# Optimization experiments

Measured on AMD Instinct MI355X. Metric: run time of the kernel, lower is better.

The kernel has to match this reference:

```python
import jax, jax.numpy as jnp
import numpy as np

F, H, D, A, B = 500, 2000, 64, 64, 4096


def setup_inputs() -> dict:
    key = jax.random.key(0)
    ks = jax.random.split(key, 6)
    values = jax.random.normal(ks[0], (B, F), dtype=jnp.float32)
    feat_emb = jax.random.normal(ks[1], (F, D), dtype=jnp.float32) * 0.02
    hid_emb = jax.random.normal(ks[2], (H, D), dtype=jnp.float32) * 0.02
    Ww = jax.random.normal(ks[3], (2 * D, A), dtype=jnp.float32) * (1.0 / np.sqrt(2 * D))
    bw = jnp.zeros((A,), dtype=jnp.float32)
    Wu = jax.random.normal(ks[4], (A, 1), dtype=jnp.float32) * (1.0 / np.sqrt(A))
    mask = jax.random.bernoulli(ks[5], 0.1, (F, F + H, 1))
    return {"values": values, "feat_emb": feat_emb, "hid_emb": hid_emb,
            "Ww": Ww, "bw": bw, "Wu": Wu, "mask": mask}


def reference(values, feat_emb, hid_emb, Ww, bw, Wu, mask):
    d = feat_emb.shape[1]
    # full embedding matrix: concat(feature, hidden) -> [F+H, d]
    full = jnp.concatenate([feat_emb, hid_emb], axis=0)
    # Dense(tanh) on concat([feat_emb tiled, full tiled], axis=2) == split-weight form:
    # avoids materializing the [F, F+H, 2d] concat tensor (same math).
    W1, W2 = Ww[:d], Ww[d:]
    pre_f = feat_emb @ W1          # [F, A]
    pre_w = full @ W2              # [F+H, A]
    h = jnp.tanh(pre_f[:, None, :] + pre_w[None, :, :] + bw)  # [F, F+H, A]
    score = h @ Wu                 # [F, F+H, 1]
    # masked exp-normalize (not a stable softmax: original uses raw exp)
    score = jnp.where(mask, jnp.exp(score), 0.0)
    ssum = jnp.sum(score, axis=1, keepdims=True)        # [F, 1, 1]
    ssum = jnp.where(ssum == 0, 1.0, ssum)
    attn = score / ssum                                  # [F, F+H, 1]
    context = jnp.sum(attn * full[None, :, :], axis=1)   # [F, d]
    return values @ context                              # [B, d]
```

## Files before the change

### kernel.cpp

```cpp
#include <hip/hip_runtime.h>
#include <cstdint>
#include <cstddef>

#define F_N 500
#define H_N 2000
#define JN  2500
#define D_N 64
#define A_N 64
#define B_N 4096

__global__ __launch_bounds__(256) void k_pre(
    const float* __restrict__ feat, const float* __restrict__ hid,
    const float* __restrict__ Ww,   const float* __restrict__ bw,
    float* __restrict__ pre_f, float* __restrict__ pre_w)
{
    const int lane = threadIdx.x & 63;
    const int wave = threadIdx.x >> 6;
    int row = blockIdx.x * 4 + wave;
    row = __builtin_amdgcn_readfirstlane(row);
    if (row >= F_N + JN) return;

    const float* emb;
    const float* W;
    float*       outp;
    float acc0, acc1 = 0.0f;

    if (row < F_N) {
        emb  = feat + (size_t)row * D_N;
        W    = Ww;
        outp = pre_f + (size_t)row * A_N;
        acc0 = bw[lane];
    } else {
        const int j = row - F_N;
        emb  = (j < F_N) ? (feat + (size_t)j * D_N)
                         : (hid + (size_t)(j - F_N) * D_N);
        W    = Ww + D_N * A_N;
        outp = pre_w + (size_t)j * A_N;
        acc0 = 0.0f;
    }

    #pragma unroll
    for (int d = 0; d < D_N; d += 2) {
        acc0 = fmaf(emb[d],     W[(d    ) * A_N + lane], acc0);
        acc1 = fmaf(emb[d + 1], W[(d + 1) * A_N + lane], acc1);
    }
    outp[lane] = acc0 + acc1;
}

__global__ __launch_bounds__(256) void k_attn(
    const float* __restrict__ feat, const float* __restrict__ hid,
    const float* __restrict__ pre_f, const float* __restrict__ pre_w,
    const float* __restrict__ Wu,   const void* __restrict__ mask,
    float* __restrict__ ctx)
{
    const int tid  = threadIdx.x;
    const int lane = tid & 63;
    const int wave = tid >> 6;
    const int i    = blockIdx.x;

    __shared__ int   list[JN];
    __shared__ float earr[JN];
    __shared__ float s_ctx[4][64];
    __shared__ int   nact;

    if (tid == 0) nact = 0;
    __syncthreads();

    const uint32_t* mw = (const uint32_t*)mask;
    const uint32_t probe = mw[lane] | mw[64 + lane] | mw[128 + lane] | mw[192 + lane];
    const bool byteMode = (__ballot(probe > 1u) != 0ull);

    const uint8_t*  mb = (const uint8_t*)mask + (size_t)i * JN;
    const uint32_t* mi = (const uint32_t*)mask + (size_t)i * JN;

    for (int t = tid; t < 2560; t += 256) {
        uint32_t m = 0;
        if (t < JN) m = byteMode ? (uint32_t)mb[t] : mi[t];
        const unsigned long long act = __ballot(m != 0);
        const int cnt = __popcll(act);
        int base = 0;
        if (lane == 0 && cnt) base = atomicAdd(&nact, cnt);
        base = __shfl(base, 0, 64);
        if (m) {
            const int rank = __popcll(act & ((1ull << lane) - 1ull));
            list[base + rank] = t;
        }
    }
    __syncthreads();
    const int n = nact;

    const float* pf = pre_f + (size_t)i * A_N;
    for (int idx = tid; idx < n; idx += 256) {
        const int j = list[idx];
        const float4* pwj = (const float4*)(pre_w + (size_t)j * A_N);
        float s = 0.0f;
        #pragma unroll
        for (int q = 0; q < 16; ++q) {
            const float4 v = pwj[q];
            const int a = q * 4;
            const float x0 = pf[a + 0] + v.x;
            const float x1 = pf[a + 1] + v.y;
            const float x2 = pf[a + 2] + v.z;
            const float x3 = pf[a + 3] + v.w;
            const float t0 = 1.0f - 2.0f / (__expf(2.0f * x0) + 1.0f);
            const float t1 = 1.0f - 2.0f / (__expf(2.0f * x1) + 1.0f);
            const float t2 = 1.0f - 2.0f / (__expf(2.0f * x2) + 1.0f);
            const float t3 = 1.0f - 2.0f / (__expf(2.0f * x3) + 1.0f);
            s = fmaf(Wu[a + 0], t0, s);
            s = fmaf(Wu[a + 1], t1, s);
            s = fmaf(Wu[a + 2], t2, s);
            s = fmaf(Wu[a + 3], t3, s);
        }
        earr[idx] = __expf(s);
    }
    __syncthreads();

    float cacc = 0.0f;
    int idx = wave;
    for (; idx + 12 < n; idx += 16) {
        const float e0 = earr[idx];      const int j0 = list[idx];
        const float e1 = earr[idx + 4];  const int j1 = list[idx + 4];
        const float e2 = earr[idx + 8];  const int j2 = list[idx + 8];
        const float e3 = earr[idx + 12]; const int j3 = list[idx + 12];
        const float* r0 = (j0 < F_N) ? (feat + (size_t)j0 * D_N) : (hid + (size_t)(j0 - F_N) * D_N);
        const float* r1 = (j1 < F_N) ? (feat + (size_t)j1 * D_N) : (hid + (size_t)(j1 - F_N) * D_N);
        const float* r2 = (j2 < F_N) ? (feat + (size_t)j2 * D_N) : (hid + (size_t)(j2 - F_N) * D_N);
        const float* r3 = (j3 < F_N) ? (feat + (size_t)j3 * D_N) : (hid + (size_t)(j3 - F_N) * D_N);
        const float v0 = r0[lane];
        const float v1 = r1[lane];
        const float v2 = r2[lane];
        const float v3 = r3[lane];
        cacc = fmaf(e0, v0, cacc);
        cacc = fmaf(e1, v1, cacc);
        cacc = fmaf(e2, v2, cacc);
        cacc = fmaf(e3, v3, cacc);
    }
    for (; idx < n; idx += 4) {
        const float e = earr[idx];
        const int   j = list[idx];
        const float* row = (j < F_N) ? (feat + (size_t)j * D_N)
                                     : (hid + (size_t)(j - F_N) * D_N);
        cacc = fmaf(e, row[lane], cacc);
    }
    s_ctx[wave][lane] = cacc;
    __syncthreads();

    if (wave == 0) {
        const float c4 = s_ctx[0][lane] + s_ctx[1][lane] + s_ctx[2][lane] + s_ctx[3][lane];
        float ss = 0.0f;
        for (int k = lane; k < n; k += 64) ss += earr[k];
        #pragma unroll
        for (int off = 1; off < 64; off <<= 1) ss += __shfl_xor(ss, off, 64);
        if (ss == 0.0f) ss = 1.0f;
        ctx[(size_t)i * D_N + lane] = c4 / ss;
    }
}

__global__ __launch_bounds__(256) void k_out(
    const float* __restrict__ values, const float* __restrict__ ctx,
    float* __restrict__ out)
{
    const int tid  = threadIdx.x;
    const int lane = tid & 63;
    const int wave = tid >> 6;
    const int rowB = blockIdx.x * 16;
    const int r0   = wave * 4;

    __shared__ float ctx_l[100 * 64];
    __shared__ float vals_l[16 * 100];

    float4 cbuf[7];
    float4 vbuf[2];

    float acc0 = 0.0f, acc1 = 0.0f, acc2 = 0.0f, acc3 = 0.0f;

    {
        const float4* cp = (const float4*)(ctx);
        #pragma unroll
        for (int q = 0; q < 7; ++q) {
            const int t = tid + q * 256;
            if (t < 1600) cbuf[q] = cp[t];
        }
        #pragma unroll
        for (int q = 0; q < 2; ++q) {
            const int t = tid + q * 256;
            if (t < 400) {
                const int r = t / 25, c = t % 25;
                vbuf[q] = *(const float4*)(values + (size_t)(rowB + r) * 500 + c * 4);
            }
        }
    }

    for (int chunk = 0; chunk < 5; ++chunk) {
        __syncthreads();
        {
            float4* cl = (float4*)ctx_l;
            #pragma unroll
            for (int q = 0; q < 7; ++q) {
                const int t = tid + q * 256;
                if (t < 1600) cl[t] = cbuf[q];
            }
            float4* vl = (float4*)vals_l;
            #pragma unroll
            for (int q = 0; q < 2; ++q) {
                const int t = tid + q * 256;
                if (t < 400) vl[t] = vbuf[q];
            }
        }
        __syncthreads();

        if (chunk < 4) {
            const int k0 = (chunk + 1) * 100;
            const float4* cp = (const float4*)(ctx + (size_t)k0 * 64);
            #pragma unroll
            for (int q = 0; q < 7; ++q) {
                const int t = tid + q * 256;
                if (t < 1600) cbuf[q] = cp[t];
            }
            #pragma unroll
            for (int q = 0; q < 2; ++q) {
                const int t = tid + q * 256;
                if (t < 400) {
                    const int r = t / 25, c = t % 25;
                    vbuf[q] = *(const float4*)(values + (size_t)(rowB + r) * 500 + k0 + c * 4);
                }
            }
        }

        const float* v0 = vals_l + (r0 + 0) * 100;
        const float* v1 = vals_l + (r0 + 1) * 100;
        const float* v2 = vals_l + (r0 + 2) * 100;
        const float* v3 = vals_l + (r0 + 3) * 100;
        #pragma unroll 5
        for (int k = 0; k < 100; k += 4) {
            const float4 a = *(const float4*)(v0 + k);
            const float4 b = *(const float4*)(v1 + k);
            const float4 c = *(const float4*)(v2 + k);
            const float4 d = *(const float4*)(v3 + k);
            const float c0 = ctx_l[(k + 0) * 64 + lane];
            const float c1 = ctx_l[(k + 1) * 64 + lane];
            const float c2 = ctx_l[(k + 2) * 64 + lane];
            const float c3 = ctx_l[(k + 3) * 64 + lane];
            acc0 = fmaf(a.x, c0, acc0); acc0 = fmaf(a.y, c1, acc0);
            acc0 = fmaf(a.z, c2, acc0); acc0 = fmaf(a.w, c3, acc0);
            acc1 = fmaf(b.x, c0, acc1); acc1 = fmaf(b.y, c1, acc1);
            acc1 = fmaf(b.z, c2, acc1); acc1 = fmaf(b.w, c3, acc1);
            acc2 = fmaf(c.x, c0, acc2); acc2 = fmaf(c.y, c1, acc2);
            acc2 = fmaf(c.z, c2, acc2); acc2 = fmaf(c.w, c3, acc2);
            acc3 = fmaf(d.x, c0, acc3); acc3 = fmaf(d.y, c1, acc3);
            acc3 = fmaf(d.z, c2, acc3); acc3 = fmaf(d.w, c3, acc3);
        }
    }

    const int gr = rowB + r0;
    out[(size_t)(gr + 0) * 64 + lane] = acc0;
    out[(size_t)(gr + 1) * 64 + lane] = acc1;
    out[(size_t)(gr + 2) * 64 + lane] = acc2;
    out[(size_t)(gr + 3) * 64 + lane] = acc3;
}

extern "C" void kernel_launch(void* const* d_in, const int* in_sizes, int n_in,
                              void* d_out, int out_size, void* d_ws, size_t ws_size,
                              hipStream_t stream)
{
    const float* values = (const float*)d_in[0];
    const float* feat   = (const float*)d_in[1];
    const float* hid    = (const float*)d_in[2];
    const float* Ww     = (const float*)d_in[3];
    const float* bw     = (const float*)d_in[4];
    const float* Wu     = (const float*)d_in[5];
    const void*  mask   = d_in[6];
    float* out = (float*)d_out;

    float* wsf   = (float*)d_ws;
    float* pre_f = wsf;
    float* pre_w = wsf + 32000;
    float* ctx   = wsf + 192000;

    k_pre <<<750, 256, 0, stream>>>(feat, hid, Ww, bw, pre_f, pre_w);
    k_attn<<<500, 256, 0, stream>>>(feat, hid, pre_f, pre_w, Wu, mask, ctx);
    k_out <<<256, 256, 0, stream>>>(values, ctx, out);
}
```

Baseline: 129.3 us.

## Fuse attention and output kernels with a software grid barrier

Merges the attention-context kernel and the final values@context kernel into one persistent launch of 256 blocks. The first 250 blocks each handle two feature rows, then a spin-based global barrier waits until all of ctx is written before the output GEMM phase starts. The barrier counter is reset by the preceding k_pre kernel. The tanh division is also replaced by a hardware reciprocal. This removes one launch and its inter-kernel gap, but it halves the parallelism of the attention phase, adds barrier spin cost, and relies on all 256 blocks being co-resident.

```diff
diff --git a/kernel.cpp b/kernel.cpp
--- a/kernel.cpp
+++ b/kernel.cpp
@@ -8,12 +8,16 @@
 #define D_N 64
 #define A_N 64
 #define B_N 4096
+#define NB_FUSED 256
 
 __global__ __launch_bounds__(256) void k_pre(
     const float* __restrict__ feat, const float* __restrict__ hid,
     const float* __restrict__ Ww,   const float* __restrict__ bw,
-    float* __restrict__ pre_f, float* __restrict__ pre_w)
+    float* __restrict__ pre_f, float* __restrict__ pre_w,
+    int* __restrict__ barrier_ws)
 {
+    if (blockIdx.x == 0 && threadIdx.x < 2) barrier_ws[threadIdx.x] = 0;
+
     const int lane = threadIdx.x & 63;
     const int wave = threadIdx.x >> 6;
     int row = blockIdx.x * 4 + wave;
@@ -47,171 +51,160 @@
     outp[lane] = acc0 + acc1;
 }
 
-__global__ __launch_bounds__(256) void k_attn(
+__device__ __forceinline__ void grid_barrier(int* __restrict__ ctr,
+                                             int* __restrict__ gen,
+                                             int nblocks)
+{
+    __syncthreads();
+    if (threadIdx.x == 0) {
+        __threadfence();
+        const int g = __hip_atomic_load(gen, __ATOMIC_RELAXED,
+                                        __HIP_MEMORY_SCOPE_AGENT);
+        const int old = __hip_atomic_fetch_add(ctr, 1, __ATOMIC_ACQ_REL,
+                                               __HIP_MEMORY_SCOPE_AGENT);
+        if (old == nblocks - 1) {
+            __hip_atomic_store(gen, g + 1, __ATOMIC_RELEASE,
+                               __HIP_MEMORY_SCOPE_AGENT);
+        } else {
+            while (__hip_atomic_load(gen, __ATOMIC_ACQUIRE,
+                                     __HIP_MEMORY_SCOPE_AGENT) == g) {
+                __builtin_amdgcn_s_sleep(2);
+            }
+        }
+    }
+    __syncthreads();
+}
+
+__global__ __launch_bounds__(256) void k_fused(
     const float* __restrict__ feat, const float* __restrict__ hid,
     const float* __restrict__ pre_f, const float* __restrict__ pre_w,
     const float* __restrict__ Wu,   const void* __restrict__ mask,
-    float* __restrict__ ctx)
+    const float* __restrict__ values,
+    float* __restrict__ ctx, float* __restrict__ out,
+    int* __restrict__ barrier_ws)
 {
     const int tid  = threadIdx.x;
     const int lane = tid & 63;
     const int wave = tid >> 6;
-    const int i    = blockIdx.x;
 
     __shared__ int   list[JN];
     __shared__ float earr[JN];
     __shared__ float s_ctx[4][64];
     __shared__ int   nact;
-
-    if (tid == 0) nact = 0;
-    __syncthreads();
-
-    const uint32_t* mw = (const uint32_t*)mask;
-    const uint32_t probe = mw[lane] | mw[64 + lane] | mw[128 + lane] | mw[192 + lane];
-    const bool byteMode = (__ballot(probe > 1u) != 0ull);
-
-    const uint8_t*  mb = (const uint8_t*)mask + (size_t)i * JN;
-    const uint32_t* mi = (const uint32_t*)mask + (size_t)i * JN;
-
-    for (int t = tid; t < 2560; t += 256) {
-        uint32_t m = 0;
-        if (t < JN) m = byteMode ? (uint32_t)mb[t] : mi[t];
-        const unsigned long long act = __ballot(m != 0);
-        const int cnt = __popcll(act);
-        int base = 0;
-        if (lane == 0 && cnt) base = atomicAdd(&nact, cnt);
-        base = __shfl(base, 0, 64);
-        if (m) {
-            const int rank = __popcll(act & ((1ull << lane) - 1ull));
-            list[base + rank] = t;
-        }
-    }
-    __syncthreads();
-    const int n = nact;
-
-    const float* pf = pre_f + (size_t)i * A_N;
-    for (int idx = tid; idx < n; idx += 256) {
-        const int j = list[idx];
-        const float4* pwj = (const float4*)(pre_w + (size_t)j * A_N);
-        float s = 0.0f;
-        #pragma unroll
-        for (int q = 0; q < 16; ++q) {
-            const float4 v = pwj[q];
-            const int a = q * 4;
-            const float x0 = pf[a + 0] + v.x;
-            const float x1 = pf[a + 1] + v.y;
-            const float x2 = pf[a + 2] + v.z;
-            const float x3 = pf[a + 3] + v.w;
-            const float t0 = 1.0f - 2.0f / (__expf(2.0f * x0) + 1.0f);
-            const float t1 = 1.0f - 2.0f / (__expf(2.0f * x1) + 1.0f);
-            const float t2 = 1.0f - 2.0f / (__expf(2.0f * x2) + 1.0f);
-            const float t3 = 1.0f - 2.0f / (__expf(2.0f * x3) + 1.0f);
-            s = fmaf(Wu[a + 0], t0, s);
-            s = fmaf(Wu[a + 1], t1, s);
-            s = fmaf(Wu[a + 2], t2, s);
-            s = fmaf(Wu[a + 3], t3, s);
-        }
-        earr[idx] = __expf(s);
-    }
-    __syncthreads();
-
-    float cacc = 0.0f;
-    int idx = wave;
-    for (; idx + 12 < n; idx += 16) {
-        const float e0 = earr[idx];      const int j0 = list[idx];
-        const float e1 = earr[idx + 4];  const int j1 = list[idx + 4];
-        const float e2 = earr[idx + 8];  const int j2 = list[idx + 8];
-        const float e3 = earr[idx + 12]; const int j3 = list[idx + 12];
-        const float* r0 = (j0 < F_N) ? (feat + (size_t)j0 * D_N) : (hid + (size_t)(j0 - F_N) * D_N);
-        const float* r1 = (j1 < F_N) ? (feat + (size_t)j1 * D_N) : (hid + (size_t)(j1 - F_N) * D_N);
-        const float* r2 = (j2 < F_N) ? (feat + (size_t)j2 * D_N) : (hid + (size_t)(j2 - F_N) * D_N);
-        const float* r3 = (j3 < F_N) ? (feat + (size_t)j3 * D_N) : (hid + (size_t)(j3 - F_N) * D_N);
-        const float v0 = r0[lane];
-        const float v1 = r1[lane];
-        const float v2 = r2[lane];
-        const float v3 = r3[lane];
-        cacc = fmaf(e0, v0, cacc);
-        cacc = fmaf(e1, v1, cacc);
-        cacc = fmaf(e2, v2, cacc);
-        cacc = fmaf(e3, v3, cacc);
-    }
-    for (; idx < n; idx += 4) {
-        const float e = earr[idx];
-        const int   j = list[idx];
-        const float* row = (j < F_N) ? (feat + (size_t)j * D_N)
-                                     : (hid + (size_t)(j - F_N) * D_N);
-        cacc = fmaf(e, row[lane], cacc);
-    }
-    s_ctx[wave][lane] = cacc;
-    __syncthreads();
-
-    if (wave == 0) {
-        const float c4 = s_ctx[0][lane] + s_ctx[1][lane] + s_ctx[2][lane] + s_ctx[3][lane];
-        float ss = 0.0f;
-        for (int k = lane; k < n; k += 64) ss += earr[k];
-        #pragma unroll
-        for (int off = 1; off < 64; off <<= 1) ss += __shfl_xor(ss, off, 64);
-        if (ss == 0.0f) ss = 1.0f;
-        ctx[(size_t)i * D_N + lane] = c4 / ss;
-    }
-}
-
-__global__ __launch_bounds__(256) void k_out(
-    const float* __restrict__ values, const float* __restrict__ ctx,
-    float* __restrict__ out)
-{
-    const int tid  = threadIdx.x;
-    const int lane = tid & 63;
-    const int wave = tid >> 6;
-    const int rowB = blockIdx.x * 16;
-    const int r0   = wave * 4;
-
     __shared__ float ctx_l[100 * 64];
     __shared__ float vals_l[16 * 100];
 
-    float4 cbuf[7];
-    float4 vbuf[2];
-
-    float acc0 = 0.0f, acc1 = 0.0f, acc2 = 0.0f, acc3 = 0.0f;
+    if (blockIdx.x < 250) {
+        const uint32_t* mw = (const uint32_t*)mask;
+        const uint32_t probe = mw[lane] | mw[64 + lane] | mw[128 + lane] | mw[192 + lane];
+        const bool byteMode = (__ballot(probe > 1u) != 0ull);
+
+        for (int rep = 0; rep < 2; ++rep) {
+            const int i = blockIdx.x * 2 + rep;
+
+            if (tid == 0) nact = 0;
+            __syncthreads();
+
+            const uint8_t*  mb = (const uint8_t*)mask + (size_t)i * JN;
+            const uint32_t* mi = (const uint32_t*)mask + (size_t)i * JN;
+
+            for (int t = tid; t < 2560; t += 256) {
+                uint32_t m = 0;
+                if (t < JN) m = byteMode ? (uint32_t)mb[t] : mi[t];
+                const unsigned long long act = __ballot(m != 0);
+                const int cnt = __popcll(act);
+                int base = 0;
+                if (lane == 0 && cnt) base = atomicAdd(&nact, cnt);
+                base = __shfl(base, 0, 64);
+                if (m) {
+                    const int rank = __popcll(act & ((1ull << lane) - 1ull));
+                    list[base + rank] = t;
+                }
+            }
+            __syncthreads();
+            const int n = nact;
+
+            const float* pf = pre_f + (size_t)i * A_N;
+            for (int idx = tid; idx < n; idx += 256) {
+                const int j = list[idx];
+                const float4* pwj = (const float4*)(pre_w + (size_t)j * A_N);
+                float s = 0.0f;
+                #pragma unroll
+                for (int q = 0; q < 16; ++q) {
+                    const float4 v = pwj[q];
+                    const int a = q * 4;
+                    const float x0 = pf[a + 0] + v.x;
+                    const float x1 = pf[a + 1] + v.y;
+                    const float x2 = pf[a + 2] + v.z;
+                    const float x3 = pf[a + 3] + v.w;
+                    const float t0 = fmaf(-2.0f, __builtin_amdgcn_rcpf(__expf(2.0f * x0) + 1.0f), 1.0f);
+                    const float t1 = fmaf(-2.0f, __builtin_amdgcn_rcpf(__expf(2.0f * x1) + 1.0f), 1.0f);
+                    const float t2 = fmaf(-2.0f, __builtin_amdgcn_rcpf(__expf(2.0f * x2) + 1.0f), 1.0f);
+                    const float t3 = fmaf(-2.0f, __builtin_amdgcn_rcpf(__expf(2.0f * x3) + 1.0f), 1.0f);
+                    s = fmaf(Wu[a + 0], t0, s);
+                    s = fmaf(Wu[a + 1], t1, s);
+                    s = fmaf(Wu[a + 2], t2, s);
+                    s = fmaf(Wu[a + 3], t3, s);
+                }
+                earr[idx] = __expf(s);
+            }
+            __syncthreads();
+
+            float cacc = 0.0f;
+            int idx = wave;
+            for (; idx + 12 < n; idx += 16) {
+                const float e0 = earr[idx];      const int j0 = list[idx];
+                const float e1 = earr[idx + 4];  const int j1 = list[idx + 4];
+                const float e2 = earr[idx + 8];  const int j2 = list[idx + 8];
+                const float e3 = earr[idx + 12]; const int j3 = list[idx + 12];
+                const float* r0 = (j0 < F_N) ? (feat + (size_t)j0 * D_N) : (hid + (size_t)(j0 - F_N) * D_N);
+                const float* r1 = (j1 < F_N) ? (feat + (size_t)j1 * D_N) : (hid + (size_t)(j1 - F_N) * D_N);
+                const float* r2 = (j2 < F_N) ? (feat + (size_t)j2 * D_N) : (hid + (size_t)(j2 - F_N) * D_N);
+                const float* r3 = (j3 < F_N) ? (feat + (size_t)j3 * D_N) : (hid + (size_t)(j3 - F_N) * D_N);
+                const float v0 = r0[lane];
+                const float v1 = r1[lane];
+                const float v2 = r2[lane];
+                const float v3 = r3[lane];
+                cacc = fmaf(e0, v0, cacc);
+                cacc = fmaf(e1, v1, cacc);
+                cacc = fmaf(e2, v2, cacc);
+                cacc = fmaf(e3, v3, cacc);
+            }
+            for (; idx < n; idx += 4) {
+                const float e = earr[idx];
+                const int   j = list[idx];
+                const float* row = (j < F_N) ? (feat + (size_t)j * D_N)
+                                             : (hid + (size_t)(j - F_N) * D_N);
+                cacc = fmaf(e, row[lane], cacc);
+            }
+            s_ctx[wave][lane] = cacc;
+            __syncthreads();
+
+            if (wave == 0) {
+                const float c4 = s_ctx[0][lane] + s_ctx[1][lane] + s_ctx[2][lane] + s_ctx[3][lane];
+                float ss = 0.0f;
+                for (int k = lane; k < n; k += 64) ss += earr[k];
+                #pragma unroll
+                for (int off = 1; off < 64; off <<= 1) ss += __shfl_xor(ss, off, 64);
+                if (ss == 0.0f) ss = 1.0f;
+                ctx[(size_t)i * D_N + lane] = c4 / ss;
+            }
+        }
+    }
+
+    grid_barrier(barrier_ws + 0, barrier_ws + 1, NB_FUSED);
 
     {
-        const float4* cp = (const float4*)(ctx);
-        #pragma unroll
-        for (int q = 0; q < 7; ++q) {
-            const int t = tid + q * 256;
-            if (t < 1600) cbuf[q] = cp[t];
-        }
-        #pragma unroll
-        for (int q = 0; q < 2; ++q) {
-            const int t = tid + q * 256;
-            if (t < 400) {
-                const int r = t / 25, c = t % 25;
-                vbuf[q] = *(const float4*)(values + (size_t)(rowB + r) * 500 + c * 4);
-            }
-        }
-    }
-
-    for (int chunk = 0; chunk < 5; ++chunk) {
-        __syncthreads();
+        const int rowB = blockIdx.x * 16;
+        const int r0   = wave * 4;
+
+        float4 cbuf[7];
+        float4 vbuf[2];
+
+        float acc0 = 0.0f, acc1 = 0.0f, acc2 = 0.0f, acc3 = 0.0f;
+
         {
-            float4* cl = (float4*)ctx_l;
-            #pragma unroll
-            for (int q = 0; q < 7; ++q) {
-                const int t = tid + q * 256;
-                if (t < 1600) cl[t] = cbuf[q];
-            }
-            float4* vl = (float4*)vals_l;
-            #pragma unroll
-            for (int q = 0; q < 2; ++q) {
-                const int t = tid + q * 256;
-                if (t < 400) vl[t] = vbuf[q];
-            }
-        }
-        __syncthreads();
-
-        if (chunk < 4) {
-            const int k0 = (chunk + 1) * 100;
-            const float4* cp = (const float4*)(ctx + (size_t)k0 * 64);
+            const float4* cp = (const float4*)(ctx);
             #pragma unroll
             for (int q = 0; q < 7; ++q) {
                 const int t = tid + q * 256;
@@ -222,41 +215,78 @@
                 const int t = tid + q * 256;
                 if (t < 400) {
                     const int r = t / 25, c = t % 25;
-                    vbuf[q] = *(const float4*)(values + (size_t)(rowB + r) * 500 + k0 + c * 4);
+                    vbuf[q] = *(const float4*)(values + (size_t)(rowB + r) * 500 + c * 4);
                 }
             }
         }
 
-        const float* v0 = vals_l + (r0 + 0) * 100;
-        const float* v1 = vals_l + (r0 + 1) * 100;
-        const float* v2 = vals_l + (r0 + 2) * 100;
-        const float* v3 = vals_l + (r0 + 3) * 100;
-        #pragma unroll 5
-        for (int k = 0; k < 100; k += 4) {
-            const float4 a = *(const float4*)(v0 + k);
-            const float4 b = *(const float4*)(v1 + k);
-            const float4 c = *(const float4*)(v2 + k);
-            const float4 d = *(const float4*)(v3 + k);
-            const float c0 = ctx_l[(k + 0) * 64 + lane];
-            const float c1 = ctx_l[(k + 1) * 64 + lane];
-            const float c2 = ctx_l[(k + 2) * 64 + lane];
-            const float c3 = ctx_l[(k + 3) * 64 + lane];
-            acc0 = fmaf(a.x, c0, acc0); acc0 = fmaf(a.y, c1, acc0);
-            acc0 = fmaf(a.z, c2, acc0); acc0 = fmaf(a.w, c3, acc0);
-            acc1 = fmaf(b.x, c0, acc1); acc1 = fmaf(b.y, c1, acc1);
-            acc1 = fmaf(b.z, c2, acc1); acc1 = fmaf(b.w, c3, acc1);
-            acc2 = fmaf(c.x, c0, acc2); acc2 = fmaf(c.y, c1, acc2);
-            acc2 = fmaf(c.z, c2, acc2); acc2 = fmaf(c.w, c3, acc2);
-            acc3 = fmaf(d.x, c0, acc3); acc3 = fmaf(d.y, c1, acc3);
-            acc3 = fmaf(d.z, c2, acc3); acc3 = fmaf(d.w, c3, acc3);
+        for (int chunk = 0; chunk < 5; ++chunk) {
+            __syncthreads();
+            {
+                float4* cl = (float4*)ctx_l;
+                #pragma unroll
+                for (int q = 0; q < 7; ++q) {
+                    const int t = tid + q * 256;
+                    if (t < 1600) cl[t] = cbuf[q];
+                }
+                float4* vl = (float4*)vals_l;
+                #pragma unroll
+                for (int q = 0; q < 2; ++q) {
+                    const int t = tid + q * 256;
+                    if (t < 400) vl[t] = vbuf[q];
+                }
+            }
+            __syncthreads();
+
+            if (chunk < 4) {
+                const int k0 = (chunk + 1) * 100;
+                const float4* cp = (const float4*)(ctx + (size_t)k0 * 64);
+                #pragma unroll
+                for (int q = 0; q < 7; ++q) {
+                    const int t = tid + q * 256;
+                    if (t < 1600) cbuf[q] = cp[t];
+                }
+                #pragma unroll
+                for (int q = 0; q < 2; ++q) {
+                    const int t = tid + q * 256;
+                    if (t < 400) {
+                        const int r = t / 25, c = t % 25;
+                        vbuf[q] = *(const float4*)(values + (size_t)(rowB + r) * 500 + k0 + c * 4);
+                    }
+                }
+            }
+
+            const float* v0 = vals_l + (r0 + 0) * 100;
+            const float* v1 = vals_l + (r0 + 1) * 100;
+            const float* v2 = vals_l + (r0 + 2) * 100;
+            const float* v3 = vals_l + (r0 + 3) * 100;
+            #pragma unroll 5
+            for (int k = 0; k < 100; k += 4) {
+                const float4 a = *(const float4*)(v0 + k);
+                const float4 b = *(const float4*)(v1 + k);
+                const float4 c = *(const float4*)(v2 + k);
+                const float4 d = *(const float4*)(v3 + k);
+                const float c0 = ctx_l[(k + 0) * 64 + lane];
+                const float c1 = ctx_l[(k + 1) * 64 + lane];
+                const float c2 = ctx_l[(k + 2) * 64 + lane];
+                const float c3 = ctx_l[(k + 3) * 64 + lane];
+                acc0 = fmaf(a.x, c0, acc0); acc0 = fmaf(a.y, c1, acc0);
+                acc0 = fmaf(a.z, c2, acc0); acc0 = fmaf(a.w, c3, acc0);
+                acc1 = fmaf(b.x, c0, acc1); acc1 = fmaf(b.y, c1, acc1);
+                acc1 = fmaf(b.z, c2, acc1); acc1 = fmaf(b.w, c3, acc1);
+                acc2 = fmaf(c.x, c0, acc2); acc2 = fmaf(c.y, c1, acc2);
+                acc2 = fmaf(c.z, c2, acc2); acc2 = fmaf(c.w, c3, acc2);
+                acc3 = fmaf(d.x, c0, acc3); acc3 = fmaf(d.y, c1, acc3);
+                acc3 = fmaf(d.z, c2, acc3); acc3 = fmaf(d.w, c3, acc3);
+            }
         }
-    }
-
-    const int gr = rowB + r0;
-    out[(size_t)(gr + 0) * 64 + lane] = acc0;
-    out[(size_t)(gr + 1) * 64 + lane] = acc1;
-    out[(size_t)(gr + 2) * 64 + lane] = acc2;
-    out[(size_t)(gr + 3) * 64 + lane] = acc3;
+
+        const int gr = rowB + r0;
+        out[(size_t)(gr + 0) * 64 + lane] = acc0;
+        out[(size_t)(gr + 1) * 64 + lane] = acc1;
+        out[(size_t)(gr + 2) * 64 + lane] = acc2;
+        out[(size_t)(gr + 3) * 64 + lane] = acc3;
+    }
 }
 
 extern "C" void kernel_launch(void* const* d_in, const int* in_sizes, int n_in,
@@ -276,8 +306,9 @@
     float* pre_f = wsf;
     float* pre_w = wsf + 32000;
     float* ctx   = wsf + 192000;
-
-    k_pre <<<750, 256, 0, stream>>>(feat, hid, Ww, bw, pre_f, pre_w);
-    k_attn<<<500, 256, 0, stream>>>(feat, hid, pre_f, pre_w, Wu, mask, ctx);
-    k_out <<<256, 256, 0, stream>>>(values, ctx, out);
+    int*   bar   = (int*)(wsf + 224000);
+
+    k_pre  <<<750, 256, 0, stream>>>(feat, hid, Ww, bw, pre_f, pre_w, bar);
+    k_fused<<<NB_FUSED, 256, 0, stream>>>(feat, hid, pre_f, pre_w, Wu, mask,
+                                          values, ctx, out, bar);
 }
```

Result: slower. 181.9 us (+40.6%).

## Split attention over two column chunks with atomic partial sums, defer normalization

Applied to the files above, without the earlier changes.

The attention kernel now runs two blocks per feature row, each handling half of the F+H columns. Partial context and exp sums are accumulated with float atomics into buffers that k_pre zeroes, and normalization moves into the output GEMM's LDS staging. The tanh uses a hardware reciprocal instead of a divide. k_out now reads values directly from global memory with 2 rows per wave and 512 blocks, dropping the values LDS staging. The aim is more blocks and occupancy on the latency-bound attention stage, at the cost of atomics and nondeterministic summation order, and the output GEMM loses its register reuse across rows.

```diff
diff --git a/kernel.cpp b/kernel.cpp
--- a/kernel.cpp
+++ b/kernel.cpp
@@ -9,11 +9,18 @@
 #define A_N 64
 #define B_N 4096
 
+#define SPLIT  2
+#define JCHUNK 1250
+
 __global__ __launch_bounds__(256) void k_pre(
     const float* __restrict__ feat, const float* __restrict__ hid,
     const float* __restrict__ Ww,   const float* __restrict__ bw,
-    float* __restrict__ pre_f, float* __restrict__ pre_w)
-{
+    float* __restrict__ pre_f, float* __restrict__ pre_w,
+    float* __restrict__ zero_region)
+{
+    const int gt = blockIdx.x * 256 + threadIdx.x;
+    if (gt < 32512) zero_region[gt] = 0.0f;
+
     const int lane = threadIdx.x & 63;
     const int wave = threadIdx.x >> 6;
     int row = blockIdx.x * 4 + wave;
@@ -51,15 +58,17 @@
     const float* __restrict__ feat, const float* __restrict__ hid,
     const float* __restrict__ pre_f, const float* __restrict__ pre_w,
     const float* __restrict__ Wu,   const void* __restrict__ mask,
-    float* __restrict__ ctx)
+    float* __restrict__ csum, float* __restrict__ esum)
 {
     const int tid  = threadIdx.x;
     const int lane = tid & 63;
     const int wave = tid >> 6;
-    const int i    = blockIdx.x;
-
-    __shared__ int   list[JN];
-    __shared__ float earr[JN];
+    const int i    = blockIdx.x >> 1;
+    const int sub  = blockIdx.x & 1;
+    const int jbase = sub * JCHUNK;
+
+    __shared__ int   list[JCHUNK];
+    __shared__ float earr[JCHUNK];
     __shared__ float s_ctx[4][64];
     __shared__ int   nact;
 
@@ -70,12 +79,12 @@
     const uint32_t probe = mw[lane] | mw[64 + lane] | mw[128 + lane] | mw[192 + lane];
     const bool byteMode = (__ballot(probe > 1u) != 0ull);
 
-    const uint8_t*  mb = (const uint8_t*)mask + (size_t)i * JN;
-    const uint32_t* mi = (const uint32_t*)mask + (size_t)i * JN;
-
-    for (int t = tid; t < 2560; t += 256) {
+    const uint8_t*  mb = (const uint8_t*)mask + (size_t)i * JN + jbase;
+    const uint32_t* mi = (const uint32_t*)mask + (size_t)i * JN + jbase;
+
+    for (int t = tid; t < 1280; t += 256) {
         uint32_t m = 0;
-        if (t < JN) m = byteMode ? (uint32_t)mb[t] : mi[t];
+        if (t < JCHUNK) m = byteMode ? (uint32_t)mb[t] : mi[t];
         const unsigned long long act = __ballot(m != 0);
         const int cnt = __popcll(act);
         int base = 0;
@@ -83,7 +92,7 @@
         base = __shfl(base, 0, 64);
         if (m) {
             const int rank = __popcll(act & ((1ull << lane) - 1ull));
-            list[base + rank] = t;
+            list[base + rank] = jbase + t;
         }
     }
     __syncthreads();
@@ -102,10 +111,10 @@
             const float x1 = pf[a + 1] + v.y;
             const float x2 = pf[a + 2] + v.z;
             const float x3 = pf[a + 3] + v.w;
-            const float t0 = 1.0f - 2.0f / (__expf(2.0f * x0) + 1.0f);
-            const float t1 = 1.0f - 2.0f / (__expf(2.0f * x1) + 1.0f);
-            const float t2 = 1.0f - 2.0f / (__expf(2.0f * x2) + 1.0f);
-            const float t3 = 1.0f - 2.0f / (__expf(2.0f * x3) + 1.0f);
+            const float t0 = fmaf(-2.0f, __builtin_amdgcn_rcpf(__expf(2.0f * x0) + 1.0f), 1.0f);
+            const float t1 = fmaf(-2.0f, __builtin_amdgcn_rcpf(__expf(2.0f * x1) + 1.0f), 1.0f);
+            const float t2 = fmaf(-2.0f, __builtin_amdgcn_rcpf(__expf(2.0f * x2) + 1.0f), 1.0f);
+            const float t3 = fmaf(-2.0f, __builtin_amdgcn_rcpf(__expf(2.0f * x3) + 1.0f), 1.0f);
             s = fmaf(Wu[a + 0], t0, s);
             s = fmaf(Wu[a + 1], t1, s);
             s = fmaf(Wu[a + 2], t2, s);
@@ -151,43 +160,34 @@
         for (int k = lane; k < n; k += 64) ss += earr[k];
         #pragma unroll
         for (int off = 1; off < 64; off <<= 1) ss += __shfl_xor(ss, off, 64);
-        if (ss == 0.0f) ss = 1.0f;
-        ctx[(size_t)i * D_N + lane] = c4 / ss;
+        atomicAdd(&csum[(size_t)i * D_N + lane], c4);
+        if (lane == 0) atomicAdd(&esum[i], ss);
     }
 }
 
 __global__ __launch_bounds__(256) void k_out(
-    const float* __restrict__ values, const float* __restrict__ ctx,
-    float* __restrict__ out)
+    const float* __restrict__ values, const float* __restrict__ csum,
+    const float* __restrict__ esum,   float* __restrict__ out)
 {
     const int tid  = threadIdx.x;
     const int lane = tid & 63;
     const int wave = tid >> 6;
-    const int rowB = blockIdx.x * 16;
-    const int r0   = wave * 4;
+    int r0 = blockIdx.x * 8 + wave * 2;
+    r0 = __builtin_amdgcn_readfirstlane(r0);
 
     __shared__ float ctx_l[100 * 64];
-    __shared__ float vals_l[16 * 100];
 
     float4 cbuf[7];
-    float4 vbuf[2];
-
-    float acc0 = 0.0f, acc1 = 0.0f, acc2 = 0.0f, acc3 = 0.0f;
+    float  ebuf[7];
+
+    float acc0 = 0.0f, acc1 = 0.0f;
 
     {
-        const float4* cp = (const float4*)(ctx);
+        const float4* cp = (const float4*)csum;
         #pragma unroll
         for (int q = 0; q < 7; ++q) {
             const int t = tid + q * 256;
-            if (t < 1600) cbuf[q] = cp[t];
-        }
-        #pragma unroll
-        for (int q = 0; q < 2; ++q) {
-            const int t = tid + q * 256;
-            if (t < 400) {
-                const int r = t / 25, c = t % 25;
-                vbuf[q] = *(const float4*)(values + (size_t)(rowB + r) * 500 + c * 4);
-            }
+            if (t < 1600) { cbuf[q] = cp[t]; ebuf[q] = esum[t >> 4]; }
         }
     }
 
@@ -198,65 +198,45 @@
             #pragma unroll
             for (int q = 0; q < 7; ++q) {
                 const int t = tid + q * 256;
-                if (t < 1600) cl[t] = cbuf[q];
+                if (t < 1600) {
+                    const float e   = ebuf[q];
+                    const float inv = (e == 0.0f) ? 1.0f : __builtin_amdgcn_rcpf(e);
+                    float4 c = cbuf[q];
+                    c.x *= inv; c.y *= inv; c.z *= inv; c.w *= inv;
+                    cl[t] = c;
+                }
             }
-            float4* vl = (float4*)vals_l;
-            #pragma unroll
-            for (int q = 0; q < 2; ++q) {
-                const int t = tid + q * 256;
-                if (t < 400) vl[t] = vbuf[q];
-            }
         }
         __syncthreads();
 
         if (chunk < 4) {
-            const int k0 = (chunk + 1) * 100;
-            const float4* cp = (const float4*)(ctx + (size_t)k0 * 64);
+            const int k0n = (chunk + 1) * 100;
+            const float4* cp = (const float4*)(csum + (size_t)k0n * 64);
             #pragma unroll
             for (int q = 0; q < 7; ++q) {
                 const int t = tid + q * 256;
-                if (t < 1600) cbuf[q] = cp[t];
+                if (t < 1600) { cbuf[q] = cp[t]; ebuf[q] = esum[k0n + (t >> 4)]; }
             }
-            #pragma unroll
-            for (int q = 0; q < 2; ++q) {
-                const int t = tid + q * 256;
-                if (t < 400) {
-                    const int r = t / 25, c = t % 25;
-                    vbuf[q] = *(const float4*)(values + (size_t)(rowB + r) * 500 + k0 + c * 4);
-                }
-            }
-        }
-
-        const float* v0 = vals_l + (r0 + 0) * 100;
-        const float* v1 = vals_l + (r0 + 1) * 100;
-        const float* v2 = vals_l + (r0 + 2) * 100;
-        const float* v3 = vals_l + (r0 + 3) * 100;
-        #pragma unroll 5
+        }
+
+        const int k0 = chunk * 100;
+        const float* v0 = values + (size_t)(r0 + 0) * 500 + k0;
+        const float* v1 = values + (size_t)(r0 + 1) * 500 + k0;
+        #pragma unroll 10
         for (int k = 0; k < 100; k += 4) {
-            const float4 a = *(const float4*)(v0 + k);
-            const float4 b = *(const float4*)(v1 + k);
-            const float4 c = *(const float4*)(v2 + k);
-            const float4 d = *(const float4*)(v3 + k);
             const float c0 = ctx_l[(k + 0) * 64 + lane];
             const float c1 = ctx_l[(k + 1) * 64 + lane];
             const float c2 = ctx_l[(k + 2) * 64 + lane];
             const float c3 = ctx_l[(k + 3) * 64 + lane];
-            acc0 = fmaf(a.x, c0, acc0); acc0 = fmaf(a.y, c1, acc0);
-            acc0 = fmaf(a.z, c2, acc0); acc0 = fmaf(a.w, c3, acc0);
-            acc1 = fmaf(b.x, c0, acc1); acc1 = fmaf(b.y, c1, acc1);
-            acc1 = fmaf(b.z, c2, acc1); acc1 = fmaf(b.w, c3, acc1);
-            acc2 = fmaf(c.x, c0, acc2); acc2 = fmaf(c.y, c1, acc2);
-            acc2 = fmaf(c.z, c2, acc2); acc2 = fmaf(c.w, c3, acc2);
-            acc3 = fmaf(d.x, c0, acc3); acc3 = fmaf(d.y, c1, acc3);
-            acc3 = fmaf(d.z, c2, acc3); acc3 = fmaf(d.w, c3, acc3);
-        }
-    }
-
-    const int gr = rowB + r0;
-    out[(size_t)(gr + 0) * 64 + lane] = acc0;
-    out[(size_t)(gr + 1) * 64 + lane] = acc1;
-    out[(size_t)(gr + 2) * 64 + lane] = acc2;
-    out[(size_t)(gr + 3) * 64 + lane] = acc3;
+            acc0 = fmaf(v0[k + 0], c0, acc0); acc0 = fmaf(v0[k + 1], c1, acc0);
+            acc0 = fmaf(v0[k + 2], c2, acc0); acc0 = fmaf(v0[k + 3], c3, acc0);
+            acc1 = fmaf(v1[k + 0], c0, acc1); acc1 = fmaf(v1[k + 1], c1, acc1);
+            acc1 = fmaf(v1[k + 2], c2, acc1); acc1 = fmaf(v1[k + 3], c3, acc1);
+        }
+    }
+
+    out[(size_t)(r0 + 0) * 64 + lane] = acc0;
+    out[(size_t)(r0 + 1) * 64 + lane] = acc1;
 }
 
 extern "C" void kernel_launch(void* const* d_in, const int* in_sizes, int n_in,
@@ -275,9 +255,10 @@
     float* wsf   = (float*)d_ws;
     float* pre_f = wsf;
     float* pre_w = wsf + 32000;
-    float* ctx   = wsf + 192000;
-
-    k_pre <<<750, 256, 0, stream>>>(feat, hid, Ww, bw, pre_f, pre_w);
-    k_attn<<<500, 256, 0, stream>>>(feat, hid, pre_f, pre_w, Wu, mask, ctx);
-    k_out <<<256, 256, 0, stream>>>(values, ctx, out);
-}
+    float* csum  = wsf + 192000;
+    float* esum  = wsf + 224000;
+
+    k_pre <<<750,  256, 0, stream>>>(feat, hid, Ww, bw, pre_f, pre_w, csum);
+    k_attn<<<1000, 256, 0, stream>>>(feat, hid, pre_f, pre_w, Wu, mask, csum, esum);
+    k_out <<<512,  256, 0, stream>>>(values, csum, esum, out);
+}
```

Measured after the change: 109.4 us (median of 2 runs). -15.4%, faster.
